# Kernel optimization log

Measured on AMD Instinct MI355X. Metric: run time of the kernel, lower is better.

The kernel has to match this reference:

```python
import jax, jax.numpy as jnp
import numpy as np

B, T, F, H = 1024, 512, 32, 64
EPS = 1e-3  # keras BatchNormalization default epsilon


def lstm_layer(x, Wx, Uh, b):
    """Keras LSTM with activation=relu, recurrent_activation=sigmoid.
    x: [B,T,Fin]; Wx: [Fin,4H]; Uh: [H,4H]; b: [4H]. Gate order i,f,c,o."""
    xz = jnp.einsum('btf,fg->btg', x, Wx) + b  # precompute input projection
    h0 = jnp.zeros((x.shape[0], Uh.shape[0]), x.dtype)

    def step(carry, xz_t):
        h, c = carry
        z = xz_t + h @ Uh
        i, f, g, o = jnp.split(z, 4, axis=-1)
        i = jax.nn.sigmoid(i)
        f = jax.nn.sigmoid(f)
        o = jax.nn.sigmoid(o)
        c = f * c + i * jax.nn.relu(g)
        h = o * jax.nn.relu(c)
        return (h, c), h

    _, hs = jax.lax.scan(step, (h0, h0), jnp.swapaxes(xz, 0, 1))  # [T,B,H]
    return jnp.swapaxes(hs, 0, 1)  # [B,T,H]


def batchnorm(x, gamma, beta, mean, var):
    # inference-mode BN over last axis (keras default axis=-1, training=False)
    return (x - mean) * (gamma * jax.lax.rsqrt(var + EPS)) + beta


def attention(x, W, ht):
    # score = (X @ W) @ h_t -> [B,T]; softmax over time; c_t = X^T @ alpha
    score = jnp.einsum('btd,de,e->bt', x, W, ht[:, 0])
    alpha = jax.nn.softmax(score, axis=1)
    return jnp.einsum('btd,bt->bd', x, alpha)  # [B,H]


def setup_inputs() -> dict:
    key = jax.random.key(0)
    ks = jax.random.split(key, 32)
    d = {'x': jax.random.normal(ks[0], (B, T, F), jnp.float32)}
    fins = [F, H, H]
    for l in range(3):
        fin = fins[l]
        i = l + 1
        d[f'w{i}'] = jax.random.normal(ks[1 + 9 * l], (fin, 4 * H), jnp.float32) * (1.0 / np.sqrt(fin))
        d[f'u{i}'] = jax.random.normal(ks[2 + 9 * l], (H, 4 * H), jnp.float32) * (1.0 / np.sqrt(H))
        d[f'bi{i}'] = jnp.zeros((4 * H,), jnp.float32)
        d[f'gamma{i}'] = jnp.ones((H,), jnp.float32)
        d[f'beta{i}'] = jnp.zeros((H,), jnp.float32)
        d[f'mean{i}'] = jax.random.normal(ks[3 + 9 * l], (H,), jnp.float32) * 0.1
        d[f'var{i}'] = jnp.ones((H,), jnp.float32) + jax.random.uniform(ks[4 + 9 * l], (H,), jnp.float32) * 0.1
        d[f'attw{i}'] = jax.random.truncated_normal(ks[5 + 9 * l], -2, 2, (H, H), jnp.float32) * 0.5
        d[f'attv{i}'] = jax.random.truncated_normal(ks[6 + 9 * l], -2, 2, (H, 1), jnp.float32) * 0.5
    d['dw'] = jax.random.normal(ks[30], (3 * H, 1), jnp.float32) * (1.0 / np.sqrt(3 * H))
    d['db'] = jnp.zeros((1,), jnp.float32)
    return d


def reference(x, w1, u1, bi1, gamma1, beta1, mean1, var1, attw1, attv1,
              w2, u2, bi2, gamma2, beta2, mean2, var2, attw2, attv2,
              w3, u3, bi3, gamma3, beta3, mean3, var3, attw3, attv3,
              dw, db):
    h = lstm_layer(x, w1, u1, bi1)
    h = batchnorm(h, gamma1, beta1, mean1, var1)
    a1 = attention(h, attw1, attv1)
    h = lstm_layer(h, w2, u2, bi2)
    h = batchnorm(h, gamma2, beta2, mean2, var2)
    a2 = attention(h, attw2, attv2)
    h = lstm_layer(h, w3, u3, bi3)
    h = batchnorm(h, gamma3, beta3, mean3, var3)
    a3 = attention(h, attw3, attv3)
    feat = jnp.concatenate([a1, a2, a3], axis=1)  # [B, 3H]
    return feat @ dw + db  # [B, 1]
```

## Files before the change

kernel.cpp:

```cpp
#include <hip/hip_runtime.h>
#include <math.h>

#define BB 1024
#define TT 512
#define FF 32
#define HH 64
#define GG 256
#define TC 64
#define NCHUNK (TT/TC)
#define MB 16
#define NBLK (BB/MB)
#define HPAD 68
#define EPSBN 1e-3f

typedef __attribute__((ext_vector_type(8))) short bf16x8;
typedef __attribute__((ext_vector_type(4))) float f32x4;
typedef __attribute__((ext_vector_type(4))) int   i32x4;
typedef unsigned short ushort_t;

__global__ void fold1_kernel(const float* __restrict__ gamma, const float* __restrict__ beta,
                             const float* __restrict__ mean, const float* __restrict__ var,
                             const float* __restrict__ attw, const float* __restrict__ attv,
                             float* __restrict__ s_out, float* __restrict__ ab_out,
                             float* __restrict__ wv_out) {
    int d = threadIdx.x;
    float s = gamma[d] * rsqrtf(var[d] + EPSBN);
    float ab = beta[d] - mean[d] * s;
    float wvr = 0.f;
    for (int e = 0; e < HH; ++e) wvr += attw[d * HH + e] * attv[e];
    s_out[d] = s;
    ab_out[d] = ab;
    wv_out[d] = s * wvr;
}

__global__ void fold2_kernel(const float* __restrict__ W, const float* __restrict__ b,
                             const float* __restrict__ s_prev, const float* __restrict__ ab_prev,
                             float* __restrict__ Wp, float* __restrict__ bp) {
    int g = threadIdx.x;
    float bacc = b[g];
    for (int d = 0; d < HH; ++d) {
        float w = W[d * GG + g];
        bacc += ab_prev[d] * w;
        Wp[d * GG + g] = s_prev[d] * w;
    }
    bp[g] = bacc;
}

__global__ void init_kernel(float* st_h, float* st_c, float* st_acc, float* st_m, float* st_d) {
    int i = blockIdx.x * blockDim.x + threadIdx.x;
    int n = 3 * BB * HH;
    if (i < n) { st_h[i] = 0.f; st_c[i] = 0.f; st_acc[i] = 0.f; }
    if (i < 3 * BB) { st_m[i] = -3.0e38f; st_d[i] = 0.f; }
}

__device__ __forceinline__ f32x4 ld4(const float* p) { return *reinterpret_cast<const f32x4*>(p); }
__device__ __forceinline__ void st4(float* p, f32x4 v) { *reinterpret_cast<f32x4*>(p) = v; }
__device__ __forceinline__ int cvtpk(float a, float b) {
    int r; asm("v_cvt_pk_bf16_f32 %0, %1, %2" : "=v"(r) : "v"(a), "v"(b)); return r;
}
__device__ __forceinline__ void mkfrag(f32x4 A, f32x4 B, bf16x8& hi, bf16x8& lo) {
    i32x4 H, L;
    H[0] = cvtpk(A[0], A[1]); H[1] = cvtpk(A[2], A[3]);
    H[2] = cvtpk(B[0], B[1]); H[3] = cvtpk(B[2], B[3]);
    L[0] = cvtpk(A[0] - __int_as_float(H[0] << 16), A[1] - __int_as_float(H[0] & 0xffff0000));
    L[1] = cvtpk(A[2] - __int_as_float(H[1] << 16), A[3] - __int_as_float(H[1] & 0xffff0000));
    L[2] = cvtpk(B[0] - __int_as_float(H[2] << 16), B[1] - __int_as_float(H[2] & 0xffff0000));
    L[3] = cvtpk(B[2] - __int_as_float(H[3] << 16), B[3] - __int_as_float(H[3] & 0xffff0000));
    hi = __builtin_bit_cast(bf16x8, H); lo = __builtin_bit_cast(bf16x8, L);
}
__device__ __forceinline__ float sigm(float x) { return __fdividef(1.f, 1.f + __expf(-x)); }
#define MFMA(a, b, c) c = __builtin_amdgcn_mfma_f32_16x16x32_bf16(a, b, c, 0, 0, 0)
#define PIN(x) asm volatile("" : "+v"(x))

__global__ void prep_frags(const float* __restrict__ M, int KT, ushort_t* __restrict__ outF) {
    int idx = blockIdx.x * 256 + threadIdx.x;
    int tot = 16 * KT * 512;
    if (idx >= tot) return;
    int e = idx & 7, l = (idx >> 3) & 63, f = idx >> 9;
    int kt = f % KT, gw = f / KT;
    int g = gw & 3, w = gw >> 2;
    int r = l & 15, q = l >> 4;
    int k = 32 * kt + 8 * q + e;
    int col = 64 * g + 16 * w + r;
    float v = M[(size_t)k * GG + col];
    int hb = cvtpk(v, v) & 0xffff;
    float hf = __int_as_float(hb << 16);
    float lo = v - hf;
    int lb = cvtpk(lo, lo) & 0xffff;
    outF[(size_t)(f * 2 + 0) * 512 + l * 8 + e] = (ushort_t)hb;
    outF[(size_t)(f * 2 + 1) * 512 + l * 8 + e] = (ushort_t)lb;
}

struct RecFArgs {
    const float* xin[3]; long sB[3]; long sT[3]; int K[3];
    const ushort_t* UF[3]; const ushort_t* WF[3]; const float* bias[3];
    float* Hout[3];
    float* st_h[3]; float* st_c[3]; float* st_acc[3];
    float* st_m[3]; float* st_d[3];
    const float* wv[3]; const float* abv[3]; const float* sbn[3];
    float* a_out[3];
    int last[3]; int first[3];
};

template<int KT>
__device__ __forceinline__ void rec_body(const RecFArgs& A, const int seg, const int b0,
                                         float (*hl)[MB][HPAD]) {
    const int tid = threadIdx.x;
    const int w = tid >> 6;
    const int l = tid & 63;
    const int r = l & 15;
    const int q = l >> 4;
    const int cw = w << 4;
    const int grow = b0 + r;

    const bf16x8* UF = reinterpret_cast<const bf16x8*>(A.UF[seg]);
    const bf16x8* WF = reinterpret_cast<const bf16x8*>(A.WF[seg]);
#define LDU(g,kt,hl_) UF[(((((w<<2)+(g))*2+(kt))*2)+(hl_))*64 + l]
#define LDW(g,kt,hl_) WF[(((((w<<2)+(g))*KT+(kt))*2)+(hl_))*64 + l]
    bf16x8 uh00=LDU(0,0,0), uh01=LDU(0,1,0), uh10=LDU(1,0,0), uh11=LDU(1,1,0),
           uh20=LDU(2,0,0), uh21=LDU(2,1,0), uh30=LDU(3,0,0), uh31=LDU(3,1,0);
    bf16x8 ul00=LDU(0,0,1), ul01=LDU(0,1,1), ul10=LDU(1,0,1), ul11=LDU(1,1,1),
           ul20=LDU(2,0,1), ul21=LDU(2,1,1), ul30=LDU(3,0,1), ul31=LDU(3,1,1);
    bf16x8 wh00=LDW(0,0,0), wh10=LDW(1,0,0), wh20=LDW(2,0,0), wh30=LDW(3,0,0);
    bf16x8 wl00=LDW(0,0,1), wl10=LDW(1,0,1), wl20=LDW(2,0,1), wl30=LDW(3,0,1);
    bf16x8 wh01{}, wh11{}, wh21{}, wh31{}, wl01{}, wl11{}, wl21{}, wl31{};
    if constexpr (KT == 2) {
        wh01=LDW(0,1,0); wh11=LDW(1,1,0); wh21=LDW(2,1,0); wh31=LDW(3,1,0);
        wl01=LDW(0,1,1); wl11=LDW(1,1,1); wl21=LDW(2,1,1); wl31=LDW(3,1,1);
    }
    PIN(uh00);PIN(uh01);PIN(uh10);PIN(uh11);PIN(uh20);PIN(uh21);PIN(uh30);PIN(uh31);
    PIN(ul00);PIN(ul01);PIN(ul10);PIN(ul11);PIN(ul20);PIN(ul21);PIN(ul30);PIN(ul31);
    PIN(wh00);PIN(wh10);PIN(wh20);PIN(wh30);
    PIN(wl00);PIN(wl10);PIN(wl20);PIN(wl30);
    if constexpr (KT == 2) {
        PIN(wh01);PIN(wh11);PIN(wh21);PIN(wh31);
        PIN(wl01);PIN(wl11);PIN(wl21);PIN(wl31);
    }

    f32x4 bias40 = ld4(A.bias[seg] +   0 + cw + 4 * q);
    f32x4 bias41 = ld4(A.bias[seg] +  64 + cw + 4 * q);
    f32x4 bias42 = ld4(A.bias[seg] + 128 + cw + 4 * q);
    f32x4 bias43 = ld4(A.bias[seg] + 192 + cw + 4 * q);
    f32x4 wva = ld4(A.wv[seg] + 8 * q);
    f32x4 wvb = ld4(A.wv[seg] + 8 * q + 4);
    f32x4 wvc = ld4(A.wv[seg] + 32 + 8 * q);
    f32x4 wvd = ld4(A.wv[seg] + 32 + 8 * q + 4);

    f32x4 c4   = ld4(A.st_c[seg]   + (size_t)grow * HH + cw + 4 * q);
    f32x4 h4   = ld4(A.st_h[seg]   + (size_t)grow * HH + cw + 4 * q);
    f32x4 acc4 = ld4(A.st_acc[seg] + (size_t)grow * HH + cw + 4 * q);
    float m_b = A.st_m[seg][grow];
    float d_b = A.st_d[seg][grow];

    st4(&hl[0][r][cw + 4 * q], h4);

    const float* xbase = A.xin[seg] + (size_t)grow * A.sB[seg];
    const long sT = A.sT[seg];

    f32x4 x0, x1, x2{}, x3{};
    {
        const float* xp = xbase + 8 * q;
        x0 = ld4(xp); x1 = ld4(xp + 4);
        if constexpr (KT == 2) { x2 = ld4(xp + 32); x3 = ld4(xp + 36); }
    }
    __syncthreads();

    const bool first = A.first[seg] != 0;
    float* Hob = A.Hout[seg];

#pragma unroll 2
    for (int t = 0; t < TC; ++t) {
        const int pr = t & 1;
        const int tn = (t + 1 < TC) ? t + 1 : TC - 1;
        const float* xp = xbase + (size_t)tn * sT + 8 * q;
        f32x4 n0 = ld4(xp), n1 = ld4(xp + 4), n2{}, n3{};
        if constexpr (KT == 2) { n2 = ld4(xp + 32); n3 = ld4(xp + 36); }

        f32x4 f0 = ld4(&hl[pr][r][8 * q]);
        f32x4 f1 = ld4(&hl[pr][r][8 * q + 4]);
        f32x4 f2 = ld4(&hl[pr][r][32 + 8 * q]);
        f32x4 f3 = ld4(&hl[pr][r][32 + 8 * q + 4]);
        f32x4 hp4 = ld4(&hl[pr][r][cw + 4 * q]);

        bf16x8 bh0, bl0, bh1, bl1, xh0, xl0, xh1, xl1;
        mkfrag(f0, f1, bh0, bl0);
        mkfrag(f2, f3, bh1, bl1);
        mkfrag(x0, x1, xh0, xl0);
        if constexpr (KT == 2) mkfrag(x2, x3, xh1, xl1);

        f32x4 C0 = bias40;
        MFMA(wh00, xh0, C0); MFMA(wh00, xl0, C0); MFMA(wl00, xh0, C0);
        if constexpr (KT == 2) { MFMA(wh01, xh1, C0); MFMA(wh01, xl1, C0); MFMA(wl01, xh1, C0); }
        MFMA(uh00, bh0, C0); MFMA(uh00, bl0, C0); MFMA(ul00, bh0, C0);
        MFMA(uh01, bh1, C0); MFMA(uh01, bl1, C0); MFMA(ul01, bh1, C0);
        f32x4 C1 = bias41;
        MFMA(wh10, xh0, C1); MFMA(wh10, xl0, C1); MFMA(wl10, xh0, C1);
        if constexpr (KT == 2) { MFMA(wh11, xh1, C1); MFMA(wh11, xl1, C1); MFMA(wl11, xh1, C1); }
        MFMA(uh10, bh0, C1); MFMA(uh10, bl0, C1); MFMA(ul10, bh0, C1);
        MFMA(uh11, bh1, C1); MFMA(uh11, bl1, C1); MFMA(ul11, bh1, C1);
        f32x4 C2 = bias42;
        MFMA(wh20, xh0, C2); MFMA(wh20, xl0, C2); MFMA(wl20, xh0, C2);
        if constexpr (KT == 2) { MFMA(wh21, xh1, C2); MFMA(wh21, xl1, C2); MFMA(wl21, xh1, C2); }
        MFMA(uh20, bh0, C2); MFMA(uh20, bl0, C2); MFMA(ul20, bh0, C2);
        MFMA(uh21, bh1, C2); MFMA(uh21, bl1, C2); MFMA(ul21, bh1, C2);
        f32x4 C3 = bias43;
        MFMA(wh30, xh0, C3); MFMA(wh30, xl0, C3); MFMA(wl30, xh0, C3);
        if constexpr (KT == 2) { MFMA(wh31, xh1, C3); MFMA(wh31, xl1, C3); MFMA(wl31, xh1, C3); }
        MFMA(uh30, bh0, C3); MFMA(uh30, bl0, C3); MFMA(ul30, bh0, C3);
        MFMA(uh31, bh1, C3); MFMA(uh31, bl1, C3); MFMA(ul31, bh1, C3);

        if (!(first && t == 0)) {
            float sc = 0.f;
#pragma unroll
            for (int i = 0; i < 4; ++i) {
                sc = fmaf(f0[i], wva[i], sc);
                sc = fmaf(f1[i], wvb[i], sc);
                sc = fmaf(f2[i], wvc[i], sc);
                sc = fmaf(f3[i], wvd[i], sc);
            }
            sc += __shfl_xor(sc, 16);
            sc += __shfl_xor(sc, 32);
            float mn = fmaxf(m_b, sc);
            float corr = __expf(m_b - mn);
            float p = __expf(sc - mn);
            d_b = d_b * corr + p;
            acc4 = acc4 * corr + p * hp4;
            m_b = mn;
        }

#pragma unroll
        for (int i = 0; i < 4; ++i) {
            float zi = sigm(C0[i]);
            float zf = sigm(C1[i]);
            float zg = fmaxf(C2[i], 0.f);
            float zo = sigm(C3[i]);
            c4[i] = fmaf(zf, c4[i], zi * zg);
            h4[i] = zo * fmaxf(c4[i], 0.f);
        }
        st4(&hl[pr ^ 1][r][cw + 4 * q], h4);
        if (Hob) st4(Hob + (size_t)grow * (TC * HH) + (size_t)t * HH + cw + 4 * q, h4);

        x0 = n0; x1 = n1;
        if constexpr (KT == 2) { x2 = n2; x3 = n3; }
        __syncthreads();
    }

    if (A.last[seg]) {
        f32x4 f0 = ld4(&hl[0][r][8 * q]);
        f32x4 f1 = ld4(&hl[0][r][8 * q + 4]);
        f32x4 f2 = ld4(&hl[0][r][32 + 8 * q]);
        f32x4 f3 = ld4(&hl[0][r][32 + 8 * q + 4]);
        float sc = 0.f;
#pragma unroll
        for (int i = 0; i < 4; ++i) {
            sc = fmaf(f0[i], wva[i], sc);
            sc = fmaf(f1[i], wvb[i], sc);
            sc = fmaf(f2[i], wvc[i], sc);
            sc = fmaf(f3[i], wvd[i], sc);
        }
        sc += __shfl_xor(sc, 16);
        sc += __shfl_xor(sc, 32);
        float mn = fmaxf(m_b, sc);
        float corr = __expf(m_b - mn);
        float p = __expf(sc - mn);
        d_b = d_b * corr + p;
        acc4 = acc4 * corr + p * h4;
        m_b = mn;
        f32x4 sb = ld4(A.sbn[seg] + cw + 4 * q);
        f32x4 ab = ld4(A.abv[seg] + cw + 4 * q);
        f32x4 res;
#pragma unroll
        for (int i = 0; i < 4; ++i)
            res[i] = sb[i] * __fdividef(acc4[i], d_b) + ab[i];
        st4(A.a_out[seg] + (size_t)grow * HH + cw + 4 * q, res);
    }
    st4(A.st_c[seg]   + (size_t)grow * HH + cw + 4 * q, c4);
    st4(A.st_h[seg]   + (size_t)grow * HH + cw + 4 * q, h4);
    st4(A.st_acc[seg] + (size_t)grow * HH + cw + 4 * q, acc4);
    if (w == 0 && q == 0) { A.st_m[seg][grow] = m_b; A.st_d[seg][grow] = d_b; }
#undef LDU
#undef LDW
}

__global__ __launch_bounds__(256, 1) void rec_mfma(RecFArgs A) {
    __shared__ float hl[2][MB][HPAD];
    const int seg = blockIdx.x >> 6;
    const int b0 = (blockIdx.x & (NBLK - 1)) << 4;
    if (A.K[seg] == 32) rec_body<1>(A, seg, b0, hl);
    else                rec_body<2>(A, seg, b0, hl);
}

__global__ void final_kernel(const float* __restrict__ a, const float* __restrict__ dw,
                             const float* __restrict__ db, float* __restrict__ out) {
    int b = blockIdx.x * blockDim.x + threadIdx.x;
    if (b >= BB) return;
    float acc = db[0];
    for (int l = 0; l < 3; ++l)
        for (int j = 0; j < HH; ++j)
            acc += a[(l * BB + b) * HH + j] * dw[l * HH + j];
    out[b] = acc;
}

extern "C" void kernel_launch(void* const* d_in, const int* in_sizes, int n_in,
                              void* d_out, int out_size, void* d_ws, size_t ws_size,
                              hipStream_t stream) {
    (void)in_sizes; (void)n_in; (void)out_size; (void)ws_size;
    const float* x = (const float*)d_in[0];
    const float* w[3]    = {(const float*)d_in[1],  (const float*)d_in[10], (const float*)d_in[19]};
    const float* uu[3]   = {(const float*)d_in[2],  (const float*)d_in[11], (const float*)d_in[20]};
    const float* bi[3]   = {(const float*)d_in[3],  (const float*)d_in[12], (const float*)d_in[21]};
    const float* gam[3]  = {(const float*)d_in[4],  (const float*)d_in[13], (const float*)d_in[22]};
    const float* bet[3]  = {(const float*)d_in[5],  (const float*)d_in[14], (const float*)d_in[23]};
    const float* mea[3]  = {(const float*)d_in[6],  (const float*)d_in[15], (const float*)d_in[24]};
    const float* var[3]  = {(const float*)d_in[7],  (const float*)d_in[16], (const float*)d_in[25]};
    const float* atw[3]  = {(const float*)d_in[8],  (const float*)d_in[17], (const float*)d_in[26]};
    const float* atv[3]  = {(const float*)d_in[9],  (const float*)d_in[18], (const float*)d_in[27]};
    const float* dw = (const float*)d_in[28];
    const float* db = (const float*)d_in[29];

    float* ws = (float*)d_ws;
    size_t off = 0;
    float* Hb[2][2];
    for (int l = 0; l < 2; ++l)
        for (int p = 0; p < 2; ++p) { Hb[l][p] = ws + off; off += (size_t)BB * TC * HH; }
    float* st_h  = ws + off; off += 3 * BB * HH;
    float* st_c  = ws + off; off += 3 * BB * HH;
    float* st_ac = ws + off; off += 3 * BB * HH;
    float* st_m  = ws + off; off += 3 * BB;
    float* st_d  = ws + off; off += 3 * BB;
    float* s_ws  = ws + off; off += 3 * HH;
    float* ab_ws = ws + off; off += 3 * HH;
    float* wv_ws = ws + off; off += 3 * HH;
    float* W2p   = ws + off; off += HH * GG;
    float* W3p   = ws + off; off += HH * GG;
    float* b2p   = ws + off; off += GG;
    float* b3p   = ws + off; off += GG;
    float* a_ws  = ws + off; off += 3 * BB * HH;
    ushort_t* UFb[3]; ushort_t* WFb[3];
    for (int l = 0; l < 3; ++l) { UFb[l] = (ushort_t*)(ws + off); off += 16384; }
    for (int l = 0; l < 3; ++l) { WFb[l] = (ushort_t*)(ws + off); off += 16384; }

    for (int l = 0; l < 3; ++l)
        fold1_kernel<<<1, 64, 0, stream>>>(gam[l], bet[l], mea[l], var[l], atw[l], atv[l],
                                           s_ws + l * HH, ab_ws + l * HH, wv_ws + l * HH);
    fold2_kernel<<<1, 256, 0, stream>>>(w[1], bi[1], s_ws + 0 * HH, ab_ws + 0 * HH, W2p, b2p);
    fold2_kernel<<<1, 256, 0, stream>>>(w[2], bi[2], s_ws + 1 * HH, ab_ws + 1 * HH, W3p, b3p);
    init_kernel<<<(3 * BB * HH + 255) / 256, 256, 0, stream>>>(st_h, st_c, st_ac, st_m, st_d);

    for (int l = 0; l < 3; ++l)
        prep_frags<<<64, 256, 0, stream>>>(uu[l], 2, UFb[l]);
    prep_frags<<<32, 256, 0, stream>>>(w[0], 1, WFb[0]);
    prep_frags<<<64, 256, 0, stream>>>(W2p, 2, WFb[1]);
    prep_frags<<<64, 256, 0, stream>>>(W3p, 2, WFb[2]);

    const float* bl[3] = {bi[0], b2p, b3p};

    for (int s = 0; s <= NCHUNK - 1 + 2; ++s) {
        RecFArgs ra;
        int nseg = 0;
        for (int l = 0; l < 3; ++l) {
            int cpos = s - l;
            if (cpos < 0 || cpos >= NCHUNK) continue;
            if (l == 0) {
                ra.xin[nseg] = x + (size_t)cpos * TC * FF;
                ra.sB[nseg] = (long)TT * FF;
                ra.sT[nseg] = FF;
                ra.K[nseg] = 32;
            } else {
                ra.xin[nseg] = Hb[l - 1][(s & 1) ^ 1];
                ra.sB[nseg] = (long)TC * HH;
                ra.sT[nseg] = HH;
                ra.K[nseg] = 64;
            }
            ra.UF[nseg] = UFb[l]; ra.WF[nseg] = WFb[l]; ra.bias[nseg] = bl[l];
            ra.Hout[nseg] = (l < 2) ? Hb[l][s & 1] : (float*)0;
            ra.st_h[nseg] = st_h + l * BB * HH;
            ra.st_c[nseg] = st_c + l * BB * HH;
            ra.st_acc[nseg] = st_ac + l * BB * HH;
            ra.st_m[nseg] = st_m + l * BB;
            ra.st_d[nseg] = st_d + l * BB;
            ra.wv[nseg]  = wv_ws + l * HH;
            ra.abv[nseg] = ab_ws + l * HH;
            ra.sbn[nseg] = s_ws + l * HH;
            ra.a_out[nseg] = a_ws + l * BB * HH;
            ra.last[nseg]  = (cpos == NCHUNK - 1) ? 1 : 0;
            ra.first[nseg] = (cpos == 0) ? 1 : 0;
            ++nseg;
        }
        if (!nseg) continue;
        rec_mfma<<<nseg * NBLK, 256, 0, stream>>>(ra);
    }
    final_kernel<<<(BB + 255) / 256, 256, 0, stream>>>(a_ws, dw, db, (float*)d_out);
}
```

Measured before the change: 789.0 us.

## Precompute bf16 hi/lo planes for inputs, drop W low-part MFMAs, allow 2 blocks/CU

```diff
diff --git a/kernel.cpp b/kernel.cpp
--- a/kernel.cpp
+++ b/kernel.cpp
@@ -55,6 +55,7 @@
 
 __device__ __forceinline__ f32x4 ld4(const float* p) { return *reinterpret_cast<const f32x4*>(p); }
 __device__ __forceinline__ void st4(float* p, f32x4 v) { *reinterpret_cast<f32x4*>(p) = v; }
+__device__ __forceinline__ bf16x8 ldbf(const ushort_t* p) { return *reinterpret_cast<const bf16x8*>(p); }
 __device__ __forceinline__ int cvtpk(float a, float b) {
     int r; asm("v_cvt_pk_bf16_f32 %0, %1, %2" : "=v"(r) : "v"(a), "v"(b)); return r;
 }
@@ -70,7 +71,6 @@
 }
 __device__ __forceinline__ float sigm(float x) { return __fdividef(1.f, 1.f + __expf(-x)); }
 #define MFMA(a, b, c) c = __builtin_amdgcn_mfma_f32_16x16x32_bf16(a, b, c, 0, 0, 0)
-#define PIN(x) asm volatile("" : "+v"(x))
 
 __global__ void prep_frags(const float* __restrict__ M, int KT, ushort_t* __restrict__ outF) {
     int idx = blockIdx.x * 256 + threadIdx.x;
@@ -91,10 +91,25 @@
     outF[(size_t)(f * 2 + 1) * 512 + l * 8 + e] = (ushort_t)lb;
 }
 
+__global__ void prep_planes(const float* __restrict__ in, ushort_t* __restrict__ hi,
+                            ushort_t* __restrict__ lo, int n4) {
+    int i = blockIdx.x * 256 + threadIdx.x;
+    if (i >= n4) return;
+    f32x4 v = reinterpret_cast<const f32x4*>(in)[i];
+    int p0 = cvtpk(v[0], v[1]), p1 = cvtpk(v[2], v[3]);
+    float a0 = v[0] - __int_as_float(p0 << 16);
+    float a1 = v[1] - __int_as_float(p0 & 0xffff0000);
+    float a2 = v[2] - __int_as_float(p1 << 16);
+    float a3 = v[3] - __int_as_float(p1 & 0xffff0000);
+    int q0 = cvtpk(a0, a1), q1 = cvtpk(a2, a3);
+    reinterpret_cast<int2*>(hi)[i] = make_int2(p0, p1);
+    reinterpret_cast<int2*>(lo)[i] = make_int2(q0, q1);
+}
+
 struct RecFArgs {
-    const float* xin[3]; long sB[3]; long sT[3]; int K[3];
+    const ushort_t* xhi[3]; const ushort_t* xlo[3]; long sB[3]; long sT[3]; int K[3];
     const ushort_t* UF[3]; const ushort_t* WF[3]; const float* bias[3];
-    float* Hout[3];
+    ushort_t* Hhi[3]; ushort_t* Hlo[3];
     float* st_h[3]; float* st_c[3]; float* st_acc[3];
     float* st_m[3]; float* st_d[3];
     const float* wv[3]; const float* abv[3]; const float* sbn[3];
@@ -115,26 +130,16 @@
 
     const bf16x8* UF = reinterpret_cast<const bf16x8*>(A.UF[seg]);
     const bf16x8* WF = reinterpret_cast<const bf16x8*>(A.WF[seg]);
-#define LDU(g,kt,hl_) UF[(((((w<<2)+(g))*2+(kt))*2)+(hl_))*64 + l]
-#define LDW(g,kt,hl_) WF[(((((w<<2)+(g))*KT+(kt))*2)+(hl_))*64 + l]
+#define LDU(g,kt,p_) UF[(((((w<<2)+(g))*2+(kt))*2)+(p_))*64 + l]
+#define LDW(g,kt)    WF[(((((w<<2)+(g))*KT+(kt))*2)+0)*64 + l]
     bf16x8 uh00=LDU(0,0,0), uh01=LDU(0,1,0), uh10=LDU(1,0,0), uh11=LDU(1,1,0),
            uh20=LDU(2,0,0), uh21=LDU(2,1,0), uh30=LDU(3,0,0), uh31=LDU(3,1,0);
     bf16x8 ul00=LDU(0,0,1), ul01=LDU(0,1,1), ul10=LDU(1,0,1), ul11=LDU(1,1,1),
            ul20=LDU(2,0,1), ul21=LDU(2,1,1), ul30=LDU(3,0,1), ul31=LDU(3,1,1);
-    bf16x8 wh00=LDW(0,0,0), wh10=LDW(1,0,0), wh20=LDW(2,0,0), wh30=LDW(3,0,0);
-    bf16x8 wl00=LDW(0,0,1), wl10=LDW(1,0,1), wl20=LDW(2,0,1), wl30=LDW(3,0,1);
-    bf16x8 wh01{}, wh11{}, wh21{}, wh31{}, wl01{}, wl11{}, wl21{}, wl31{};
+    bf16x8 wh00=LDW(0,0), wh10=LDW(1,0), wh20=LDW(2,0), wh30=LDW(3,0);
+    bf16x8 wh01{}, wh11{}, wh21{}, wh31{};
     if constexpr (KT == 2) {
-        wh01=LDW(0,1,0); wh11=LDW(1,1,0); wh21=LDW(2,1,0); wh31=LDW(3,1,0);
-        wl01=LDW(0,1,1); wl11=LDW(1,1,1); wl21=LDW(2,1,1); wl31=LDW(3,1,1);
-    }
-    PIN(uh00);PIN(uh01);PIN(uh10);PIN(uh11);PIN(uh20);PIN(uh21);PIN(uh30);PIN(uh31);
-    PIN(ul00);PIN(ul01);PIN(ul10);PIN(ul11);PIN(ul20);PIN(ul21);PIN(ul30);PIN(ul31);
-    PIN(wh00);PIN(wh10);PIN(wh20);PIN(wh30);
-    PIN(wl00);PIN(wl10);PIN(wl20);PIN(wl30);
-    if constexpr (KT == 2) {
-        PIN(wh01);PIN(wh11);PIN(wh21);PIN(wh31);
-        PIN(wl01);PIN(wl11);PIN(wl21);PIN(wl31);
+        wh01=LDW(0,1); wh11=LDW(1,1); wh21=LDW(2,1); wh31=LDW(3,1);
     }
 
     f32x4 bias40 = ld4(A.bias[seg] +   0 + cw + 4 * q);
@@ -154,58 +159,53 @@
 
     st4(&hl[0][r][cw + 4 * q], h4);
 
-    const float* xbase = A.xin[seg] + (size_t)grow * A.sB[seg];
+    const ushort_t* xhib = A.xhi[seg] + (size_t)grow * A.sB[seg];
+    const ushort_t* xlob = A.xlo[seg] + (size_t)grow * A.sB[seg];
     const long sT = A.sT[seg];
 
-    f32x4 x0, x1, x2{}, x3{};
-    {
-        const float* xp = xbase + 8 * q;
-        x0 = ld4(xp); x1 = ld4(xp + 4);
-        if constexpr (KT == 2) { x2 = ld4(xp + 32); x3 = ld4(xp + 36); }
-    }
+    bf16x8 xh0 = ldbf(xhib + 8 * q), xl0 = ldbf(xlob + 8 * q);
+    bf16x8 xh1{}, xl1{};
+    if constexpr (KT == 2) { xh1 = ldbf(xhib + 32 + 8 * q); xl1 = ldbf(xlob + 32 + 8 * q); }
     __syncthreads();
 
     const bool first = A.first[seg] != 0;
-    float* Hob = A.Hout[seg];
+    ushort_t* Hhi = A.Hhi[seg];
+    ushort_t* Hlo = A.Hlo[seg];
 
 #pragma unroll 2
     for (int t = 0; t < TC; ++t) {
         const int pr = t & 1;
-        const int tn = (t + 1 < TC) ? t + 1 : TC - 1;
-        const float* xp = xbase + (size_t)tn * sT + 8 * q;
-        f32x4 n0 = ld4(xp), n1 = ld4(xp + 4), n2{}, n3{};
-        if constexpr (KT == 2) { n2 = ld4(xp + 32); n3 = ld4(xp + 36); }
-
         f32x4 f0 = ld4(&hl[pr][r][8 * q]);
         f32x4 f1 = ld4(&hl[pr][r][8 * q + 4]);
         f32x4 f2 = ld4(&hl[pr][r][32 + 8 * q]);
         f32x4 f3 = ld4(&hl[pr][r][32 + 8 * q + 4]);
-        f32x4 hp4 = ld4(&hl[pr][r][cw + 4 * q]);
-
-        bf16x8 bh0, bl0, bh1, bl1, xh0, xl0, xh1, xl1;
+        const int tn = (t + 1 < TC) ? t + 1 : TC - 1;
+        const ushort_t* xph = xhib + (size_t)tn * sT + 8 * q;
+        const ushort_t* xpl = xlob + (size_t)tn * sT + 8 * q;
+        bf16x8 nh0 = ldbf(xph), nl0 = ldbf(xpl), nh1{}, nl1{};
+        if constexpr (KT == 2) { nh1 = ldbf(xph + 32); nl1 = ldbf(xpl + 32); }
+
+        f32x4 C0 = bias40, C1 = bias41, C2 = bias42, C3 = bias43;
+        MFMA(wh00, xh0, C0); MFMA(wh00, xl0, C0);
+        MFMA(wh10, xh0, C1); MFMA(wh10, xl0, C1);
+        MFMA(wh20, xh0, C2); MFMA(wh20, xl0, C2);
+        MFMA(wh30, xh0, C3); MFMA(wh30, xl0, C3);
+        if constexpr (KT == 2) {
+            MFMA(wh01, xh1, C0); MFMA(wh01, xl1, C0);
+            MFMA(wh11, xh1, C1); MFMA(wh11, xl1, C1);
+            MFMA(wh21, xh1, C2); MFMA(wh21, xl1, C2);
+            MFMA(wh31, xh1, C3); MFMA(wh31, xl1, C3);
+        }
+
+        bf16x8 bh0, bl0, bh1, bl1;
         mkfrag(f0, f1, bh0, bl0);
         mkfrag(f2, f3, bh1, bl1);
-        mkfrag(x0, x1, xh0, xl0);
-        if constexpr (KT == 2) mkfrag(x2, x3, xh1, xl1);
-
-        f32x4 C0 = bias40;
-        MFMA(wh00, xh0, C0); MFMA(wh00, xl0, C0); MFMA(wl00, xh0, C0);
-        if constexpr (KT == 2) { MFMA(wh01, xh1, C0); MFMA(wh01, xl1, C0); MFMA(wl01, xh1, C0); }
         MFMA(uh00, bh0, C0); MFMA(uh00, bl0, C0); MFMA(ul00, bh0, C0);
         MFMA(uh01, bh1, C0); MFMA(uh01, bl1, C0); MFMA(ul01, bh1, C0);
-        f32x4 C1 = bias41;
-        MFMA(wh10, xh0, C1); MFMA(wh10, xl0, C1); MFMA(wl10, xh0, C1);
-        if constexpr (KT == 2) { MFMA(wh11, xh1, C1); MFMA(wh11, xl1, C1); MFMA(wl11, xh1, C1); }
         MFMA(uh10, bh0, C1); MFMA(uh10, bl0, C1); MFMA(ul10, bh0, C1);
         MFMA(uh11, bh1, C1); MFMA(uh11, bl1, C1); MFMA(ul11, bh1, C1);
-        f32x4 C2 = bias42;
-        MFMA(wh20, xh0, C2); MFMA(wh20, xl0, C2); MFMA(wl20, xh0, C2);
-        if constexpr (KT == 2) { MFMA(wh21, xh1, C2); MFMA(wh21, xl1, C2); MFMA(wl21, xh1, C2); }
         MFMA(uh20, bh0, C2); MFMA(uh20, bl0, C2); MFMA(ul20, bh0, C2);
         MFMA(uh21, bh1, C2); MFMA(uh21, bl1, C2); MFMA(ul21, bh1, C2);
-        f32x4 C3 = bias43;
-        MFMA(wh30, xh0, C3); MFMA(wh30, xl0, C3); MFMA(wl30, xh0, C3);
-        if constexpr (KT == 2) { MFMA(wh31, xh1, C3); MFMA(wh31, xl1, C3); MFMA(wl31, xh1, C3); }
         MFMA(uh30, bh0, C3); MFMA(uh30, bl0, C3); MFMA(ul30, bh0, C3);
         MFMA(uh31, bh1, C3); MFMA(uh31, bl1, C3); MFMA(ul31, bh1, C3);
 
@@ -224,7 +224,7 @@
             float corr = __expf(m_b - mn);
             float p = __expf(sc - mn);
             d_b = d_b * corr + p;
-            acc4 = acc4 * corr + p * hp4;
+            acc4 = acc4 * corr + p * h4;
             m_b = mn;
         }
 
@@ -238,10 +238,20 @@
             h4[i] = zo * fmaxf(c4[i], 0.f);
         }
         st4(&hl[pr ^ 1][r][cw + 4 * q], h4);
-        if (Hob) st4(Hob + (size_t)grow * (TC * HH) + (size_t)t * HH + cw + 4 * q, h4);
-
-        x0 = n0; x1 = n1;
-        if constexpr (KT == 2) { x2 = n2; x3 = n3; }
+        if (Hhi) {
+            int p0 = cvtpk(h4[0], h4[1]), p1 = cvtpk(h4[2], h4[3]);
+            float a0 = h4[0] - __int_as_float(p0 << 16);
+            float a1 = h4[1] - __int_as_float(p0 & 0xffff0000);
+            float a2 = h4[2] - __int_as_float(p1 << 16);
+            float a3 = h4[3] - __int_as_float(p1 & 0xffff0000);
+            int q0 = cvtpk(a0, a1), q1 = cvtpk(a2, a3);
+            size_t ho = (size_t)grow * (TC * HH) + (size_t)t * HH + cw + 4 * q;
+            *reinterpret_cast<int2*>(Hhi + ho) = make_int2(p0, p1);
+            *reinterpret_cast<int2*>(Hlo + ho) = make_int2(q0, q1);
+        }
+
+        xh0 = nh0; xl0 = nl0;
+        if constexpr (KT == 2) { xh1 = nh1; xl1 = nl1; }
         __syncthreads();
     }
 
@@ -282,7 +292,7 @@
 #undef LDW
 }
 
-__global__ __launch_bounds__(256, 1) void rec_mfma(RecFArgs A) {
+__global__ __launch_bounds__(256, 2) void rec_mfma(RecFArgs A) {
     __shared__ float hl[2][MB][HPAD];
     const int seg = blockIdx.x >> 6;
     const int b0 = (blockIdx.x & (NBLK - 1)) << 4;
@@ -320,9 +330,14 @@
 
     float* ws = (float*)d_ws;
     size_t off = 0;
-    float* Hb[2][2];
+    ushort_t* Hhi[2][2]; ushort_t* Hlo[2][2];
     for (int l = 0; l < 2; ++l)
-        for (int p = 0; p < 2; ++p) { Hb[l][p] = ws + off; off += (size_t)BB * TC * HH; }
+        for (int p = 0; p < 2; ++p) {
+            Hhi[l][p] = (ushort_t*)(ws + off); off += (size_t)BB * TC * HH / 2;
+            Hlo[l][p] = (ushort_t*)(ws + off); off += (size_t)BB * TC * HH / 2;
+        }
+    ushort_t* Xhi = (ushort_t*)(ws + off); off += (size_t)BB * TT * FF / 2;
+    ushort_t* Xlo = (ushort_t*)(ws + off); off += (size_t)BB * TT * FF / 2;
     float* st_h  = ws + off; off += 3 * BB * HH;
     float* st_c  = ws + off; off += 3 * BB * HH;
     float* st_ac = ws + off; off += 3 * BB * HH;
@@ -352,6 +367,10 @@
     prep_frags<<<32, 256, 0, stream>>>(w[0], 1, WFb[0]);
     prep_frags<<<64, 256, 0, stream>>>(W2p, 2, WFb[1]);
     prep_frags<<<64, 256, 0, stream>>>(W3p, 2, WFb[2]);
+    {
+        int n4 = BB * TT * FF / 4;
+        prep_planes<<<(n4 + 255) / 256, 256, 0, stream>>>(x, Xhi, Xlo, n4);
+    }
 
     const float* bl[3] = {bi[0], b2p, b3p};
 
@@ -362,18 +381,22 @@
             int cpos = s - l;
             if (cpos < 0 || cpos >= NCHUNK) continue;
             if (l == 0) {
-                ra.xin[nseg] = x + (size_t)cpos * TC * FF;
+                ra.xhi[nseg] = Xhi + (size_t)cpos * TC * FF;
+                ra.xlo[nseg] = Xlo + (size_t)cpos * TC * FF;
                 ra.sB[nseg] = (long)TT * FF;
                 ra.sT[nseg] = FF;
                 ra.K[nseg] = 32;
             } else {
-                ra.xin[nseg] = Hb[l - 1][(s & 1) ^ 1];
+                int par = (s & 1) ^ 1;
+                ra.xhi[nseg] = Hhi[l - 1][par];
+                ra.xlo[nseg] = Hlo[l - 1][par];
                 ra.sB[nseg] = (long)TC * HH;
                 ra.sT[nseg] = HH;
                 ra.K[nseg] = 64;
             }
             ra.UF[nseg] = UFb[l]; ra.WF[nseg] = WFb[l]; ra.bias[nseg] = bl[l];
-            ra.Hout[nseg] = (l < 2) ? Hb[l][s & 1] : (float*)0;
+            ra.Hhi[nseg] = (l < 2) ? Hhi[l][s & 1] : (ushort_t*)0;
+            ra.Hlo[nseg] = (l < 2) ? Hlo[l][s & 1] : (ushort_t*)0;
             ra.st_h[nseg] = st_h + l * BB * HH;
             ra.st_c[nseg] = st_c + l * BB * HH;
             ra.st_acc[nseg] = st_ac + l * BB * HH;
```

After: 819.0 us. 3.8% more time.
